# Performance work log

Measured on AMD Instinct MI355X. Metric: run time of the kernel, lower is better.

The kernel has to match this reference:

```python
import jax, jax.numpy as jnp
import numpy as np

B, C, H, W = 8, 128, 128, 128
C5 = 5 * C


def setup_inputs() -> dict:
    key = jax.random.key(0)
    ks = jax.random.split(key, 9)
    s_dw = 0.1   # depthwise weight scale
    s_pw = 0.02  # pointwise weight scale
    return {
        "x": jax.random.normal(ks[0], (B, C, H, W), jnp.float32),
        "w1": jax.random.normal(ks[1], (C5, 1, 1, 1), jnp.float32) * s_dw,
        "b1": jax.random.normal(ks[2], (C5,), jnp.float32) * 0.01,
        "w2": jax.random.normal(ks[3], (C5, 1, 3, 3), jnp.float32) * s_dw,
        "b2": jax.random.normal(ks[4], (C5,), jnp.float32) * 0.01,
        "w3": jax.random.normal(ks[5], (C5, 1, 3, 3), jnp.float32) * s_dw,
        "b3": jax.random.normal(ks[6], (C5,), jnp.float32) * 0.01,
        "w4": jax.random.normal(ks[7], (C, C5, 1, 1), jnp.float32) * s_pw,
        "b4": jax.random.normal(ks[8], (C,), jnp.float32) * 0.01,
    }


def nnstacking(x):
    # pad H,W by 1 then stack the 4-neighborhood + center along channels -> 5C
    p = jnp.pad(x, ((0, 0), (0, 0), (1, 1), (1, 1)))
    return jnp.concatenate(
        [p[:, :, 2:, 1:-1],   # neighbor below (i+1, j)
         p[:, :, :-2, 1:-1],  # neighbor above (i-1, j)
         p[:, :, 1:-1, 2:],   # neighbor right (i, j+1)
         p[:, :, 1:-1, :-2],  # neighbor left  (i, j-1)
         p[:, :, 1:-1, 1:-1]],  # center
        axis=1)


def _conv(x, w, b, dilation, padding, groups):
    y = jax.lax.conv_general_dilated(
        x, w, window_strides=(1, 1),
        padding=[(padding, padding), (padding, padding)],
        rhs_dilation=(dilation, dilation),
        dimension_numbers=("NCHW", "OIHW", "NCHW"),
        feature_group_count=groups)
    return y + b[None, :, None, None]


def reference(x, w1, b1, w2, b2, w3, b3, w4, b4):
    shortcut = x
    s = nnstacking(x)  # (B, 5C, H, W)
    # three depthwise branches (groups = 5C): 1x1 rate-1, 3x3 dil-8, 3x3 dil-12
    y = (_conv(s, w1, b1, 1, 0, C5)
         + _conv(s, w2, b2, 8, 8, C5)
         + _conv(s, w3, b3, 12, 12, C5))
    # pointwise 5C -> C, then residual add
    return _conv(y, w4, b4, 1, 0, 1) + shortcut
```

## Files before the change

kernel.cpp:

```cpp
#include <hip/hip_runtime.h>
#include <stdint.h>
#include <stddef.h>


static constexpr int Cc  = 128;
static constexpr int C5  = 640;
static constexpr int Hh  = 128;
static constexpr int Ww  = 128;
static constexpr int LC  = 160;
static constexpr int GR  = 42;
static constexpr int PSz = GR * LC + 8;

typedef __attribute__((ext_vector_type(8))) short short8;
typedef __attribute__((ext_vector_type(4))) float f32x4;

__device__ __forceinline__ uint16_t f2bf(float f) {
  uint32_t b = __float_as_uint(f);
  b += 0x7fffu + ((b >> 16) & 1u);
  return (uint16_t)(b >> 16);
}
__device__ __forceinline__ float bflo(uint32_t v) { return __uint_as_float(v << 16); }
__device__ __forceinline__ float bfhi(uint32_t v) { return __uint_as_float(v & 0xffff0000u); }

__device__ __forceinline__ void async16(uint16_t* lds, const uint16_t* gm) {
  __builtin_amdgcn_global_load_lds(
      (const __attribute__((address_space(1))) uint32_t*)gm,
      (__attribute__((address_space(3))) uint32_t*)lds, 16, 0, 0);
}

__global__ void prep_kernel(const float* __restrict__ w1, const float* __restrict__ b1,
                            const float* __restrict__ w2, const float* __restrict__ b2,
                            const float* __restrict__ w3, const float* __restrict__ b3,
                            const float* __restrict__ w4,
                            uint16_t* __restrict__ w4b, float* __restrict__ cw2,
                            float* __restrict__ cw3, float* __restrict__ bsum) {
  int i = blockIdx.x * 256 + threadIdx.x;
  if (i < Cc * C5) w4b[i] = f2bf(w4[i]);
  if (i < C5) {
    bsum[i] = b1[i] + b2[i] + b3[i];
#pragma unroll
    for (int t = 0; t < 9; ++t) {
      float a = w2[i * 9 + t];
      if (t == 4) a += w1[i] + w3[i * 9 + 4];
      cw2[i * 9 + t] = a;
      cw3[i * 9 + t] = w3[i * 9 + t];
    }
  }
}

__global__ __launch_bounds__(256, 2) void dw_kernel(
    const float* __restrict__ x, const float* __restrict__ cw2,
    const float* __restrict__ cw3, const float* __restrict__ bsum,
    uint16_t* __restrict__ y, int b0) {
  __shared__ uint16_t xs[4 * PSz];

  const int band = blockIdx.x;
  const int g    = blockIdx.y;
  const int bl   = blockIdx.z;
  const int bb   = b0 + bl;
  const int i0   = band * 16;
  const int tid  = threadIdx.x;

#pragma unroll
  for (int it = 0; it < 27; ++it) {
    int idx = it * 256 + tid;
    if (idx < 6720) {
      int col4 = idx % 40;
      int rr   = (idx / 40) % 42;
      int cel  = idx / 1680;
      int gi = i0 - 13 + rr;
      int gj = col4 * 4 - 16;
      float4 v = make_float4(0.f, 0.f, 0.f, 0.f);
      if ((unsigned)gi < 128u && col4 >= 4 && col4 < 36) {
        v = *(const float4*)(x + (((size_t)(bb * Cc + g * 4 + cel) * Hh + gi) << 7) + gj);
      }
      ushort4 h;
      h.x = f2bf(v.x); h.y = f2bf(v.y); h.z = f2bf(v.z); h.w = f2bf(v.w);
      *(ushort4*)(xs + cel * PSz + rr * LC + col4 * 4) = h;
    }
  }
  __syncthreads();

  const int ce = tid & 3;
  const int jt = (tid >> 2) & 7;
  const int ir = tid >> 5;
  const int j0 = jt * 16;
  const int c  = g * 4 + ce;

  float rb[48];
#define LOAD_RB(ROW)                                                      \
  do {                                                                    \
    const uint16_t* _p = xs + ce * PSz + (ROW) * LC + j0;                 \
    _Pragma("unroll") for (int _u = 0; _u < 6; ++_u) {                    \
      uint4 _q = *(const uint4*)(_p + _u * 8);                            \
      rb[_u * 8 + 0] = bflo(_q.x); rb[_u * 8 + 1] = bfhi(_q.x);           \
      rb[_u * 8 + 2] = bflo(_q.y); rb[_u * 8 + 3] = bfhi(_q.y);           \
      rb[_u * 8 + 4] = bflo(_q.z); rb[_u * 8 + 5] = bfhi(_q.z);           \
      rb[_u * 8 + 6] = bflo(_q.w); rb[_u * 8 + 7] = bfhi(_q.w);           \
    }                                                                     \
  } while (0)

  {
    float w2r[3][9], w3r[3][9], bs[3];
    const int msA[3] = {4, 2, 3};
#pragma unroll
    for (int mi = 0; mi < 3; ++mi) {
      int k = msA[mi] * Cc + c;
#pragma unroll
      for (int t = 0; t < 9; ++t) {
        w2r[mi][t] = cw2[k * 9 + t];
        w3r[mi][t] = cw3[k * 9 + t];
      }
      bs[mi] = bsum[k];
    }

#pragma unroll
    for (int it2 = 0; it2 < 2; ++it2) {
      const int i     = i0 + ir + 8 * it2;
      const int rbase = ir + 8 * it2 + 13;
      float acc[3][16];
#pragma unroll
      for (int mi = 0; mi < 3; ++mi)
#pragma unroll
        for (int jj = 0; jj < 16; ++jj) acc[mi][jj] = bs[mi];

#define AROW3(DLT, WARR, UB, DD)                                          \
      do {                                                                \
        LOAD_RB(rbase + (DLT));                                           \
        _Pragma("unroll") for (int mi = 0; mi < 3; ++mi) {                \
          const int aj = (mi == 0) ? 0 : ((mi == 1) ? 1 : -1);            \
          _Pragma("unroll") for (int v = 0; v < 3; ++v) {                 \
            const float w = WARR[mi][(UB) + v];                           \
            const int e = 16 + (DD) * (v - 1) + aj;                       \
            _Pragma("unroll") for (int jj = 0; jj < 16; ++jj)             \
              acc[mi][jj] += w * rb[e + jj];                              \
          }                                                               \
        }                                                                 \
      } while (0)

      AROW3(-12, w3r, 0, 12);
      if (j0 == 0)   acc[1][11] -= w3r[1][0] * rb[16];
      if (j0 == 112) acc[2][4]  -= w3r[2][2] * rb[31];

      AROW3(-8, w2r, 0, 8);
      if (j0 == 0)   acc[1][7]  -= w2r[1][0] * rb[16];
      if (j0 == 112) acc[2][8]  -= w2r[2][2] * rb[31];

      {
        LOAD_RB(rbase);
#pragma unroll
        for (int mi = 0; mi < 3; ++mi) {
          const int aj = (mi == 0) ? 0 : ((mi == 1) ? 1 : -1);
#pragma unroll
          for (int v = 0; v < 3; ++v) {
            const float w = w2r[mi][3 + v];
            const int e = 16 + 8 * (v - 1) + aj;
#pragma unroll
            for (int jj = 0; jj < 16; ++jj) acc[mi][jj] += w * rb[e + jj];
          }
          {
            const float w = w3r[mi][3]; const int e = 4 + aj;
#pragma unroll
            for (int jj = 0; jj < 16; ++jj) acc[mi][jj] += w * rb[e + jj];
          }
          {
            const float w = w3r[mi][5]; const int e = 28 + aj;
#pragma unroll
            for (int jj = 0; jj < 16; ++jj) acc[mi][jj] += w * rb[e + jj];
          }
        }
        if (j0 == 0)   { acc[1][7] -= w2r[1][3] * rb[16]; acc[1][11] -= w3r[1][3] * rb[16]; }
        if (j0 == 112) { acc[2][8] -= w2r[2][5] * rb[31]; acc[2][4]  -= w3r[2][5] * rb[31]; }
      }

      AROW3(8, w2r, 6, 8);
      if (j0 == 0)   acc[1][7]  -= w2r[1][6] * rb[16];
      if (j0 == 112) acc[2][8]  -= w2r[2][8] * rb[31];

      AROW3(12, w3r, 6, 12);
      if (j0 == 0)   acc[1][11] -= w3r[1][6] * rb[16];
      if (j0 == 112) acc[2][4]  -= w3r[2][8] * rb[31];
#undef AROW3

#pragma unroll
      for (int mi = 0; mi < 3; ++mi) {
        const int msA_[3] = {4, 2, 3};
        int k4 = msA_[mi] * 32 + g;
        size_t base = (((size_t)(bl * 160 + k4) << 14) + (size_t)i * Ww + j0) * 4 + ce;
#pragma unroll
        for (int jj = 0; jj < 16; ++jj) y[base + jj * 4] = f2bf(acc[mi][jj]);
      }
    }
  }

  {
    float w2r[2][9], w3r[2][9], bs[2];
#pragma unroll
    for (int mi = 0; mi < 2; ++mi) {
      int k = mi * Cc + c;
#pragma unroll
      for (int t = 0; t < 9; ++t) {
        w2r[mi][t] = cw2[k * 9 + t];
        w3r[mi][t] = cw3[k * 9 + t];
      }
      bs[mi] = bsum[k];
    }

#pragma unroll
    for (int it2 = 0; it2 < 2; ++it2) {
      const int i     = i0 + ir + 8 * it2;
      const int rbase = ir + 8 * it2 + 13;
      float acc[2][16];
#pragma unroll
      for (int mi = 0; mi < 2; ++mi)
#pragma unroll
        for (int jj = 0; jj < 16; ++jj) acc[mi][jj] = bs[mi];

#define BROW3(MI, DLT, WARR, UB, DD, BADROW)                              \
      do {                                                                \
        LOAD_RB(rbase + (DLT));                                           \
        const float sel = ((i + (DLT)) == (BADROW)) ? 0.f : 1.f;          \
        _Pragma("unroll") for (int v = 0; v < 3; ++v) {                   \
          const float w = WARR[MI][(UB) + v] * sel;                       \
          const int e = 16 + (DD) * (v - 1);                              \
          _Pragma("unroll") for (int jj = 0; jj < 16; ++jj)               \
            acc[MI][jj] += w * rb[e + jj];                                \
        }                                                                 \
      } while (0)

#define BROWC(MI, DLT, BADROW)                                            \
      do {                                                                \
        LOAD_RB(rbase + (DLT));                                           \
        const float sel = ((i + (DLT)) == (BADROW)) ? 0.f : 1.f;          \
        _Pragma("unroll") for (int v = 0; v < 3; ++v) {                   \
          const float w = w2r[MI][3 + v] * sel;                           \
          const int e = 16 + 8 * (v - 1);                                 \
          _Pragma("unroll") for (int jj = 0; jj < 16; ++jj)               \
            acc[MI][jj] += w * rb[e + jj];                                \
        }                                                                 \
        {                                                                 \
          const float w = w3r[MI][3] * sel;                               \
          _Pragma("unroll") for (int jj = 0; jj < 16; ++jj)               \
            acc[MI][jj] += w * rb[4 + jj];                                \
        }                                                                 \
        {                                                                 \
          const float w = w3r[MI][5] * sel;                               \
          _Pragma("unroll") for (int jj = 0; jj < 16; ++jj)               \
            acc[MI][jj] += w * rb[28 + jj];                               \
        }                                                                 \
      } while (0)

      BROW3(0, -11, w3r, 0, 12, 0);
      BROW3(0, -7,  w2r, 0, 8, 0);
      BROWC(0, 1, 0);
      BROW3(0, 9,   w2r, 6, 8, 0);
      BROW3(0, 13,  w3r, 6, 12, 0);
      BROW3(1, -13, w3r, 0, 12, 127);
      BROW3(1, -9,  w2r, 0, 8, 127);
      BROWC(1, -1, 127);
      BROW3(1, 7,   w2r, 6, 8, 127);
      BROW3(1, 11,  w3r, 6, 12, 127);
#undef BROW3
#undef BROWC

#pragma unroll
      for (int mi = 0; mi < 2; ++mi) {
        int k4 = mi * 32 + g;
        size_t base = (((size_t)(bl * 160 + k4) << 14) + (size_t)i * Ww + j0) * 4 + ce;
#pragma unroll
        for (int jj = 0; jj < 16; ++jj) y[base + jj * 4] = f2bf(acc[mi][jj]);
      }
    }
  }
#undef LOAD_RB
}

__global__ __launch_bounds__(256, 2) void gemm_kernel(
    const uint16_t* __restrict__ w4b, const uint16_t* __restrict__ y,
    const float* __restrict__ x, const float* __restrict__ b4,
    float* __restrict__ out, int b0) {
  __shared__ uint16_t As[2][128 * 64];
  __shared__ uint16_t Bs[2][16 * 128 * 4];

  const int tid  = threadIdx.x;
  const int lane = tid & 63;
  const int wave = tid >> 6;
  const int p0   = blockIdx.x * 128;
  const int bl   = blockIdx.y;
  const int bb   = b0 + bl;

  const int col = lane & 15;
  const int q   = lane >> 4;
  const int o_base = (wave >> 1) * 64;
  const int p_base = (wave & 1) * 64;

  f32x4 acc[4][4];
#pragma unroll
  for (int fm = 0; fm < 4; ++fm)
#pragma unroll
    for (int fn = 0; fn < 4; ++fn) acc[fm][fn] = (f32x4){0.f, 0.f, 0.f, 0.f};

#define STAGE(BUF, KT)                                                      \
  do {                                                                      \
    _Pragma("unroll") for (int l = 0; l < 4; ++l) {                         \
      int u  = (wave * 4 + l) * 64 + lane;                                  \
      int o  = u >> 3, ch = u & 7;                                          \
      async16(As[BUF] + u * 8, w4b + (size_t)o * 640 + (KT) * 64 + ch * 8); \
    }                                                                       \
    _Pragma("unroll") for (int l = 0; l < 4; ++l) {                         \
      int k4t = wave * 4 + l;                                               \
      async16(Bs[BUF] + (k4t * 64 + lane) * 8,                              \
              y + (((size_t)(bl * 160 + (KT) * 16 + k4t) << 14) + p0) * 4   \
                + lane * 8);                                                \
    }                                                                       \
  } while (0)

#define COMPUTE(BUF)                                                        \
  do {                                                                      \
    _Pragma("unroll") for (int kk = 0; kk < 2; ++kk) {                      \
      short8 af[4], bf[4];                                                  \
      _Pragma("unroll") for (int fm = 0; fm < 4; ++fm) {                    \
        int o = o_base + fm * 16 + col;                                     \
        af[fm] = *(const short8*)(As[BUF] + o * 64 + kk * 32 + q * 8);      \
      }                                                                     \
      _Pragma("unroll") for (int fn = 0; fn < 4; ++fn) {                    \
        int p = p_base + fn * 16 + col;                                     \
        union { short8 s; uint32_t u[4]; } bu;                              \
        const uint32_t* lo =                                                \
            (const uint32_t*)(Bs[BUF] + ((kk * 8 + 2 * q) * 128 + p) * 4);  \
        const uint32_t* hi =                                                \
            (const uint32_t*)(Bs[BUF] + ((kk * 8 + 2 * q + 1) * 128 + p) * 4); \
        bu.u[0] = lo[0]; bu.u[1] = lo[1]; bu.u[2] = hi[0]; bu.u[3] = hi[1]; \
        bf[fn] = bu.s;                                                      \
      }                                                                     \
      _Pragma("unroll") for (int fm = 0; fm < 4; ++fm)                      \
        _Pragma("unroll") for (int fn = 0; fn < 4; ++fn)                    \
          acc[fm][fn] = __builtin_amdgcn_mfma_f32_16x16x32_bf16(            \
              af[fm], bf[fn], acc[fm][fn], 0, 0, 0);                        \
    }                                                                       \
  } while (0)

  STAGE(0, 0);
  __syncthreads();

#pragma unroll
  for (int kt = 0; kt < 10; kt += 2) {
    STAGE(1, kt + 1);
    COMPUTE(0);
    __syncthreads();
    if (kt + 2 < 10) STAGE(0, kt + 2);
    COMPUTE(1);
    __syncthreads();
  }
#undef STAGE
#undef COMPUTE

#pragma unroll
  for (int fm = 0; fm < 4; ++fm) {
#pragma unroll
    for (int fn = 0; fn < 4; ++fn) {
      int pg = p0 + p_base + fn * 16 + col;
#pragma unroll
      for (int r = 0; r < 4; ++r) {
        int oo = o_base + fm * 16 + q * 4 + r;
        size_t oi = ((size_t)(bb * 128 + oo) << 14) + pg;
        out[oi] = acc[fm][fn][r] + b4[oo] + x[oi];
      }
    }
  }
}

extern "C" void kernel_launch(void* const* d_in, const int* in_sizes, int n_in,
                              void* d_out, int out_size, void* d_ws, size_t ws_size,
                              hipStream_t stream) {
  const float* x  = (const float*)d_in[0];
  const float* w1 = (const float*)d_in[1];
  const float* b1 = (const float*)d_in[2];
  const float* w2 = (const float*)d_in[3];
  const float* b2 = (const float*)d_in[4];
  const float* w3 = (const float*)d_in[5];
  const float* b3 = (const float*)d_in[6];
  const float* w4 = (const float*)d_in[7];
  const float* b4 = (const float*)d_in[8];
  float* out = (float*)d_out;

  char* ws = (char*)d_ws;
  uint16_t* w4b  = (uint16_t*)ws;
  float*    cw2  = (float*)(ws + 163840);
  float*    cw3  = (float*)(ws + 186880);
  float*    bsum = (float*)(ws + 209920);
  uint16_t* y    = (uint16_t*)(ws + (1 << 20));

  const size_t per_b = (size_t)160 * 16384 * 4 * 2;
  int nbc = 8;
  while (nbc > 1 && (size_t)(1 << 20) + (size_t)nbc * per_b > ws_size) nbc >>= 1;

  hipLaunchKernelGGL(prep_kernel, dim3(320), dim3(256), 0, stream,
                     w1, b1, w2, b2, w3, b3, w4, w4b, cw2, cw3, bsum);
  for (int b0 = 0; b0 < 8; b0 += nbc) {
    int nb = (8 - b0) < nbc ? (8 - b0) : nbc;
    hipLaunchKernelGGL(dw_kernel, dim3(8, 32, nb), dim3(256), 0, stream,
                       x, cw2, cw3, bsum, y, b0);
    hipLaunchKernelGGL(gemm_kernel, dim3(128, nb), dim3(256), 0, stream,
                       w4b, y, x, b4, out, b0);
  }
}
```

Baseline: 336.3 us.

## Pack bf16 outputs with lane shuffles into 16-byte vector stores

```diff
diff --git a/kernel.cpp b/kernel.cpp
--- a/kernel.cpp
+++ b/kernel.cpp
@@ -22,10 +22,69 @@
 __device__ __forceinline__ float bflo(uint32_t v) { return __uint_as_float(v << 16); }
 __device__ __forceinline__ float bfhi(uint32_t v) { return __uint_as_float(v & 0xffff0000u); }
 
+__device__ __forceinline__ uint32_t cvt_pk_bf16(float a, float b) {
+  uint32_t r;
+  asm("v_cvt_pk_bf16_f32 %0, %1, %2" : "=v"(r) : "v"(a), "v"(b));
+  return r;
+}
+
 __device__ __forceinline__ void async16(uint16_t* lds, const uint16_t* gm) {
   __builtin_amdgcn_global_load_lds(
       (const __attribute__((address_space(1))) uint32_t*)gm,
       (__attribute__((address_space(3))) uint32_t*)lds, 16, 0, 0);
+}
+
+__device__ __forceinline__ void store_pack16(uint16_t* __restrict__ dst,
+                                             int ce, const float* acc) {
+  const bool odd = (ce & 1) != 0;
+  const bool hi2 = (ce & 2) != 0;
+
+  uint32_t m[8];
+#pragma unroll
+  for (int j = 0; j < 8; ++j) m[j] = cvt_pk_bf16(acc[2 * j], acc[2 * j + 1]);
+
+  uint32_t t2[8], mp[8];
+#pragma unroll
+  for (int j = 0; j < 8; ++j) t2[j] = odd ? m[(j + 2) & 7] : m[j];
+#pragma unroll
+  for (int j = 0; j < 8; ++j) mp[j] = hi2 ? t2[(j + 4) & 7] : t2[j];
+
+  uint32_t E0 = odd ? mp[6] : mp[2];
+  uint32_t E1 = odd ? mp[7] : mp[3];
+  uint32_t E2 = odd ? mp[2] : mp[6];
+  uint32_t E3 = odd ? mp[3] : mp[7];
+  uint32_t R0 = __shfl_xor((int)E0, 1);
+  uint32_t R1 = __shfl_xor((int)E1, 1);
+  uint32_t R2 = __shfl_xor((int)E2, 1);
+  uint32_t R3 = __shfl_xor((int)E3, 1);
+
+  uint32_t O[4] = {mp[0], mp[1], mp[4], mp[5]};
+  uint32_t R[4] = {R0, R1, R2, R3};
+
+  uint32_t Q[8];
+#pragma unroll
+  for (int t = 0; t < 4; ++t) {
+    uint32_t X = odd ? R[t] : O[t];
+    uint32_t Y = odd ? O[t] : R[t];
+    Q[2 * t]     = (X & 0xffffu) | (Y << 16);
+    Q[2 * t + 1] = (X >> 16) | (Y & 0xffff0000u);
+  }
+
+  uint32_t S[4];
+#pragma unroll
+  for (int t = 0; t < 4; ++t) S[t] = __shfl_xor((int)Q[4 + t], 2);
+
+  uint32_t D[8];
+#pragma unroll
+  for (int t = 0; t < 4; ++t) {
+    D[2 * t]     = hi2 ? S[t] : Q[t];
+    D[2 * t + 1] = hi2 ? Q[t] : S[t];
+  }
+
+  uint4 v0 = make_uint4(D[0], D[1], D[2], D[3]);
+  uint4 v1 = make_uint4(D[4], D[5], D[6], D[7]);
+  *(uint4*)(dst + ce * 16)     = v0;
+  *(uint4*)(dst + ce * 16 + 8) = v1;
 }
 
 __global__ void prep_kernel(const float* __restrict__ w1, const float* __restrict__ b1,
@@ -186,9 +245,8 @@
       for (int mi = 0; mi < 3; ++mi) {
         const int msA_[3] = {4, 2, 3};
         int k4 = msA_[mi] * 32 + g;
-        size_t base = (((size_t)(bl * 160 + k4) << 14) + (size_t)i * Ww + j0) * 4 + ce;
-#pragma unroll
-        for (int jj = 0; jj < 16; ++jj) y[base + jj * 4] = f2bf(acc[mi][jj]);
+        size_t rowb = (((size_t)(bl * 160 + k4) << 14) + (size_t)i * Ww + j0) * 4;
+        store_pack16(y + rowb, ce, acc[mi]);
       }
     }
   }
@@ -266,9 +324,8 @@
 #pragma unroll
       for (int mi = 0; mi < 2; ++mi) {
         int k4 = mi * 32 + g;
-        size_t base = (((size_t)(bl * 160 + k4) << 14) + (size_t)i * Ww + j0) * 4 + ce;
-#pragma unroll
-        for (int jj = 0; jj < 16; ++jj) y[base + jj * 4] = f2bf(acc[mi][jj]);
+        size_t rowb = (((size_t)(bl * 160 + k4) << 14) + (size_t)i * Ww + j0) * 4;
+        store_pack16(y + rowb, ce, acc[mi]);
       }
     }
   }
@@ -392,7 +449,7 @@
   uint16_t* y    = (uint16_t*)(ws + (1 << 20));
 
   const size_t per_b = (size_t)160 * 16384 * 4 * 2;
-  int nbc = 8;
+  int nbc = 4;
   while (nbc > 1 && (size_t)(1 << 20) + (size_t)nbc * per_b > ws_size) nbc >>= 1;
 
   hipLaunchKernelGGL(prep_kernel, dim3(320), dim3(256), 0, stream,
```

Measured after the change: 370.6 us. 10.2% more time.
